# Performance work log

Hardware: AMD Instinct MI355X
Metric: run time of the kernel (lower is better)

## Reference

```python
import jax, jax.numpy as jnp
import numpy as np

B, T, D, L, S, SPAN = 16, 8192, 256, 256, 128, 64


def setup_inputs() -> dict:
    key = jax.random.key(0)
    k1, k2, k3, k4 = jax.random.split(key, 4)
    word_reps = jax.random.normal(k1, (B, T, D), dtype=jnp.float32)
    # contiguous non-overlapping spans of length SPAN covering each doc
    starts = jnp.arange(S, dtype=jnp.int32) * SPAN            # [S]
    ends = starts + SPAN                                      # [S]
    offsets = jnp.broadcast_to(jnp.stack([starts, ends], -1), (B, S, 2))
    W1 = jax.random.normal(k2, (D, L), dtype=jnp.float32) * (1.0 / np.sqrt(D))
    b1 = jax.random.normal(k3, (L,), dtype=jnp.float32) * 0.01
    v = jax.random.normal(k4, (L,), dtype=jnp.float32) * (1.0 / np.sqrt(L))
    return {"word_reps": word_reps, "offsets": offsets, "W1": W1, "b1": b1, "v": v}


def reference(word_reps, offsets, W1, b1, v):
    # alpha = v(start(word_reps)) : two stacked linears, no activation -> [B,T]
    alpha = jnp.einsum("btl,l->bt", jnp.einsum("btd,dl->btl", word_reps, W1) + b1, v)

    starts = offsets[..., 0]                                  # [B,S]
    ends = offsets[..., 1]                                    # [B,S]
    pos = jnp.arange(word_reps.shape[1], dtype=offsets.dtype) # [T]
    mask = (pos[None, None, :] >= starts[..., None]) & (pos[None, None, :] < ends[..., None])  # [B,S,T]

    # ragged per-span softmax over token axis
    neg_inf = jnp.asarray(-jnp.inf, dtype=alpha.dtype)
    scores = jnp.where(mask, alpha[:, None, :], neg_inf)      # [B,S,T]
    s = jax.nn.softmax(scores, axis=-1)                       # [B,S,T]

    # attention-weighted sum pooling per span
    span_rep = jnp.einsum("bst,btd->bsd", s, word_reps)       # [B,S,D]

    # span lengths phi and last-token reps
    phi = (ends - starts).astype(word_reps.dtype)[..., None]  # [B,S,1]
    batch_idx = jnp.arange(word_reps.shape[0])[:, None]       # [B,1]
    span_ends = word_reps[batch_idx, ends - 1]                # [B,S,D]

    final_span_rep = jnp.concatenate([span_ends, span_rep, phi], axis=-1)  # [B,S,2D+1]
    prop_lens = jnp.full((word_reps.shape[0],), offsets.shape[1], dtype=jnp.int32)
    return final_span_rep, prop_lens
```

## Files before the change

### kernel.cpp

```cpp
#include <hip/hip_runtime.h>
#include <math.h>

#define B_   16
#define T_   8192
#define D_   256
#define L_   256
#define S_   128

__global__ __launch_bounds__(64) void prep_weff(const float* __restrict__ W1,
                                                const float* __restrict__ v,
                                                float* __restrict__ weff) {
    int d    = blockIdx.x;
    int lane = threadIdx.x;
    const float4* w4 = reinterpret_cast<const float4*>(W1 + (size_t)d * L_);
    const float4* v4 = reinterpret_cast<const float4*>(v);
    float4 a = w4[lane];
    float4 b = v4[lane];
    float s = a.x * b.x + a.y * b.y + a.z * b.z + a.w * b.w;
#pragma unroll
    for (int off = 32; off; off >>= 1) s += __shfl_xor(s, off);
    if (lane == 0) weff[d] = s;
}

__global__ __launch_bounds__(256) void span_kernel(const float* __restrict__ wr,
                                                   const int*   __restrict__ offsets,
                                                   const float* __restrict__ weff,
                                                   float*       __restrict__ out) {
    const int tid  = threadIdx.x;
    const int wave = tid >> 6;
    const int lane = tid & 63;
    const int bs   = blockIdx.x * 4 + wave;
    const int b    = bs >> 7;
    const int sp   = bs & (S_ - 1);

    const int start = offsets[bs * 2 + 0];
    const int end   = offsets[bs * 2 + 1];
    const int len   = end - start;

    const int g  = lane >> 4;
    const int c0 = lane & 15;

    const float4* wf4 = reinterpret_cast<const float4*>(weff);
    const float4 we0 = wf4[c0];
    const float4 we1 = wf4[c0 + 16];
    const float4 we2 = wf4[c0 + 32];
    const float4 we3 = wf4[c0 + 48];

    float4 acc0 = make_float4(0.f, 0.f, 0.f, 0.f);
    float4 acc1 = make_float4(0.f, 0.f, 0.f, 0.f);
    float4 acc2 = make_float4(0.f, 0.f, 0.f, 0.f);
    float4 acc3 = make_float4(0.f, 0.f, 0.f, 0.f);
    float  z    = 0.f;

    const float* base = wr + (size_t)(b * T_ + start) * D_;

#pragma unroll 4
    for (int p = 0; p < 16; ++p) {
        const int t  = 4 * p + g;
        const int tc = (t < len) ? t : (len - 1);
        const float4* row = reinterpret_cast<const float4*>(base + (size_t)tc * D_);
        float4 x0 = row[c0];
        float4 x1 = row[c0 + 16];
        float4 x2 = row[c0 + 32];
        float4 x3 = row[c0 + 48];

        float s = x0.x * we0.x + x0.y * we0.y + x0.z * we0.z + x0.w * we0.w
                + x1.x * we1.x + x1.y * we1.y + x1.z * we1.z + x1.w * we1.w
                + x2.x * we2.x + x2.y * we2.y + x2.z * we2.z + x2.w * we2.w
                + x3.x * we3.x + x3.y * we3.y + x3.z * we3.z + x3.w * we3.w;
        s += __shfl_xor(s, 1);
        s += __shfl_xor(s, 2);
        s += __shfl_xor(s, 4);
        s += __shfl_xor(s, 8);

        const float e = (t < len) ? __expf(s) : 0.f;
        z += e;
        acc0.x += e * x0.x; acc0.y += e * x0.y; acc0.z += e * x0.z; acc0.w += e * x0.w;
        acc1.x += e * x1.x; acc1.y += e * x1.y; acc1.z += e * x1.z; acc1.w += e * x1.w;
        acc2.x += e * x2.x; acc2.y += e * x2.y; acc2.z += e * x2.z; acc2.w += e * x2.w;
        acc3.x += e * x3.x; acc3.y += e * x3.y; acc3.z += e * x3.z; acc3.w += e * x3.w;
    }

#pragma unroll
    for (int off = 16; off <= 32; off <<= 1) {
        z      += __shfl_xor(z, off);
        acc0.x += __shfl_xor(acc0.x, off); acc0.y += __shfl_xor(acc0.y, off);
        acc0.z += __shfl_xor(acc0.z, off); acc0.w += __shfl_xor(acc0.w, off);
        acc1.x += __shfl_xor(acc1.x, off); acc1.y += __shfl_xor(acc1.y, off);
        acc1.z += __shfl_xor(acc1.z, off); acc1.w += __shfl_xor(acc1.w, off);
        acc2.x += __shfl_xor(acc2.x, off); acc2.y += __shfl_xor(acc2.y, off);
        acc2.z += __shfl_xor(acc2.z, off); acc2.w += __shfl_xor(acc2.w, off);
        acc3.x += __shfl_xor(acc3.x, off); acc3.y += __shfl_xor(acc3.y, off);
        acc3.z += __shfl_xor(acc3.z, off); acc3.w += __shfl_xor(acc3.w, off);
    }
    const float inv = 1.f / z;

    const float4 sel = (g == 0) ? acc0 : (g == 1) ? acc1 : (g == 2) ? acc2 : acc3;

    const size_t o = (size_t)bs * (2 * D_ + 1);
    out[o + D_ + lane * 4 + 0] = sel.x * inv;
    out[o + D_ + lane * 4 + 1] = sel.y * inv;
    out[o + D_ + lane * 4 + 2] = sel.z * inv;
    out[o + D_ + lane * 4 + 3] = sel.w * inv;

    const float4* lrow =
        reinterpret_cast<const float4*>(wr + (size_t)(b * T_ + end - 1) * D_);
    const float4 le = lrow[lane];
    out[o + lane * 4 + 0] = le.x;
    out[o + lane * 4 + 1] = le.y;
    out[o + lane * 4 + 2] = le.z;
    out[o + lane * 4 + 3] = le.w;

    if (lane == 0) {
        out[o + 2 * D_] = (float)len;
        if (sp == 0) out[(size_t)B_ * S_ * (2 * D_ + 1) + b] = (float)S_;
    }
}

extern "C" void kernel_launch(void* const* d_in, const int* in_sizes, int n_in,
                              void* d_out, int out_size, void* d_ws, size_t ws_size,
                              hipStream_t stream) {
    const float* word_reps = (const float*)d_in[0];
    const int*   offsets   = (const int*)d_in[1];
    const float* W1        = (const float*)d_in[2];
    const float* v         = (const float*)d_in[4];
    float*       out       = (float*)d_out;
    float*       weff      = (float*)d_ws;

    prep_weff<<<D_, 64, 0, stream>>>(W1, v, weff);
    span_kernel<<<(B_ * S_) / 4, 256, 0, stream>>>(word_reps, offsets, weff, out);
}
```

Measured before the change: 33.97 us.

## Split each span across two waves and stage output rows through LDS

Each span is now handled by two waves, each covering half of its tokens, and the partial sums and normalizers are combined through shared memory. This doubles the grid and wave count so more loads are in flight on a bandwidth-bound kernel. Input rows are read with nontemporal loads. The output row is assembled in LDS and written with coalesced nontemporal stores instead of strided scalar stores. The cost is two block barriers and extra shared-memory traffic.

```diff
diff --git a/kernel.cpp b/kernel.cpp
--- a/kernel.cpp
+++ b/kernel.cpp
@@ -6,6 +6,8 @@
 #define D_   256
 #define L_   256
 #define S_   128
+
+typedef float floatx4 __attribute__((ext_vector_type(4)));
 
 __global__ __launch_bounds__(64) void prep_weff(const float* __restrict__ W1,
                                                 const float* __restrict__ v,
@@ -22,6 +24,11 @@
     if (lane == 0) weff[d] = s;
 }
 
+__device__ __forceinline__ float4 nt_load4(const float4* p) {
+    floatx4 r = __builtin_nontemporal_load(reinterpret_cast<const floatx4*>(p));
+    return make_float4(r.x, r.y, r.z, r.w);
+}
+
 __global__ __launch_bounds__(256) void span_kernel(const float* __restrict__ wr,
                                                    const int*   __restrict__ offsets,
                                                    const float* __restrict__ weff,
@@ -29,7 +36,9 @@
     const int tid  = threadIdx.x;
     const int wave = tid >> 6;
     const int lane = tid & 63;
-    const int bs   = blockIdx.x * 4 + wave;
+    const int sib  = wave >> 1;
+    const int wk   = wave & 1;
+    const int bs   = blockIdx.x * 2 + sib;
     const int b    = bs >> 7;
     const int sp   = bs & (S_ - 1);
 
@@ -54,15 +63,15 @@
 
     const float* base = wr + (size_t)(b * T_ + start) * D_;
 
-#pragma unroll 4
-    for (int p = 0; p < 16; ++p) {
-        const int t  = 4 * p + g;
+#pragma unroll
+    for (int p = 0; p < 8; ++p) {
+        const int t  = 32 * wk + 4 * p + g;
         const int tc = (t < len) ? t : (len - 1);
         const float4* row = reinterpret_cast<const float4*>(base + (size_t)tc * D_);
-        float4 x0 = row[c0];
-        float4 x1 = row[c0 + 16];
-        float4 x2 = row[c0 + 32];
-        float4 x3 = row[c0 + 48];
+        float4 x0 = nt_load4(row + c0);
+        float4 x1 = nt_load4(row + c0 + 16);
+        float4 x2 = nt_load4(row + c0 + 32);
+        float4 x3 = nt_load4(row + c0 + 48);
 
         float s = x0.x * we0.x + x0.y * we0.y + x0.z * we0.z + x0.w * we0.w
                 + x1.x * we1.x + x1.y * we1.y + x1.z * we1.z + x1.w * we1.w
@@ -93,26 +102,48 @@
         acc3.x += __shfl_xor(acc3.x, off); acc3.y += __shfl_xor(acc3.y, off);
         acc3.z += __shfl_xor(acc3.z, off); acc3.w += __shfl_xor(acc3.w, off);
     }
-    const float inv = 1.f / z;
 
     const float4 sel = (g == 0) ? acc0 : (g == 1) ? acc1 : (g == 2) ? acc2 : acc3;
 
+    __shared__ float4 sacc[4][64];
+    __shared__ float  szz[4];
+    __shared__ float  srow[2][513];
+
+    sacc[wave][lane] = sel;
+    if (lane == 0) szz[wave] = z;
+
+    float4 le = make_float4(0.f, 0.f, 0.f, 0.f);
+    if (wk == 0) {
+        const float4* lrow =
+            reinterpret_cast<const float4*>(wr + (size_t)(b * T_ + end - 1) * D_);
+        le = lrow[lane];
+    }
+    __syncthreads();
+
+    if (wk == 0) {
+        const float4 sA = sacc[2 * sib + 0][lane];
+        const float4 sB = sacc[2 * sib + 1][lane];
+        const float  inv = 1.f / (szz[2 * sib + 0] + szz[2 * sib + 1]);
+        srow[sib][lane * 4 + 0] = le.x;
+        srow[sib][lane * 4 + 1] = le.y;
+        srow[sib][lane * 4 + 2] = le.z;
+        srow[sib][lane * 4 + 3] = le.w;
+        srow[sib][256 + lane * 4 + 0] = (sA.x + sB.x) * inv;
+        srow[sib][256 + lane * 4 + 1] = (sA.y + sB.y) * inv;
+        srow[sib][256 + lane * 4 + 2] = (sA.z + sB.z) * inv;
+        srow[sib][256 + lane * 4 + 3] = (sA.w + sB.w) * inv;
+        if (lane == 0) srow[sib][512] = (float)len;
+    }
+    __syncthreads();
+
+    const int q = wk * 64 + lane;
     const size_t o = (size_t)bs * (2 * D_ + 1);
-    out[o + D_ + lane * 4 + 0] = sel.x * inv;
-    out[o + D_ + lane * 4 + 1] = sel.y * inv;
-    out[o + D_ + lane * 4 + 2] = sel.z * inv;
-    out[o + D_ + lane * 4 + 3] = sel.w * inv;
-
-    const float4* lrow =
-        reinterpret_cast<const float4*>(wr + (size_t)(b * T_ + end - 1) * D_);
-    const float4 le = lrow[lane];
-    out[o + lane * 4 + 0] = le.x;
-    out[o + lane * 4 + 1] = le.y;
-    out[o + lane * 4 + 2] = le.z;
-    out[o + lane * 4 + 3] = le.w;
-
-    if (lane == 0) {
-        out[o + 2 * D_] = (float)len;
+#pragma unroll
+    for (int k = 0; k < 4; ++k) {
+        __builtin_nontemporal_store(srow[sib][q + 128 * k], &out[o + q + 128 * k]);
+    }
+    if (q == 0) {
+        out[o + 512] = srow[sib][512];
         if (sp == 0) out[(size_t)B_ * S_ * (2 * D_ + 1) + b] = (float)S_;
     }
 }
@@ -128,5 +159,5 @@
     float*       weff      = (float*)d_ws;
 
     prep_weff<<<D_, 64, 0, stream>>>(W1, v, weff);
-    span_kernel<<<(B_ * S_) / 4, 256, 0, stream>>>(word_reps, offsets, weff, out);
+    span_kernel<<<(B_ * S_) / 2, 256, 0, stream>>>(word_reps, offsets, weff, out);
 }
```

Measured after the change: 29.92 us. 1.14x faster.

## Give each span its own 4-wave block and reduce partials through LDS

Applied to the files above, without the earlier changes.

Each block now handles one span instead of four. Each of the 4 waves processes 16 tokens, with every lane holding one float4 of a full 256-wide row, so the per-token dot product becomes a full-wave shuffle reduction. Per-wave partial softmax numerators and denominators are combined through shared memory. The last-token row is taken from the registers of the final wave, which avoids a second global read. Input rows are read with nontemporal loads and output is written with coalesced per-thread nontemporal stores; the trade-off is more blocks and two barriers per span.

```diff
diff --git a/kernel.cpp b/kernel.cpp
--- a/kernel.cpp
+++ b/kernel.cpp
@@ -6,6 +6,8 @@
 #define D_   256
 #define L_   256
 #define S_   128
+
+typedef float floatx4 __attribute__((ext_vector_type(4)));
 
 __global__ __launch_bounds__(64) void prep_weff(const float* __restrict__ W1,
                                                 const float* __restrict__ v,
@@ -22,14 +24,19 @@
     if (lane == 0) weff[d] = s;
 }
 
-__global__ __launch_bounds__(256) void span_kernel(const float* __restrict__ wr,
-                                                   const int*   __restrict__ offsets,
-                                                   const float* __restrict__ weff,
-                                                   float*       __restrict__ out) {
+__device__ __forceinline__ float4 nt_load4(const float* p) {
+    floatx4 r = __builtin_nontemporal_load(reinterpret_cast<const floatx4*>(p));
+    return make_float4(r.x, r.y, r.z, r.w);
+}
+
+__global__ __launch_bounds__(256, 8) void span_kernel(const float* __restrict__ wr,
+                                                      const int*   __restrict__ offsets,
+                                                      const float* __restrict__ weff,
+                                                      float*       __restrict__ out) {
     const int tid  = threadIdx.x;
     const int wave = tid >> 6;
     const int lane = tid & 63;
-    const int bs   = blockIdx.x * 4 + wave;
+    const int bs   = blockIdx.x;
     const int b    = bs >> 7;
     const int sp   = bs & (S_ - 1);
 
@@ -37,82 +44,60 @@
     const int end   = offsets[bs * 2 + 1];
     const int len   = end - start;
 
-    const int g  = lane >> 4;
-    const int c0 = lane & 15;
+    const float4 we = reinterpret_cast<const float4*>(weff)[lane];
 
-    const float4* wf4 = reinterpret_cast<const float4*>(weff);
-    const float4 we0 = wf4[c0];
-    const float4 we1 = wf4[c0 + 16];
-    const float4 we2 = wf4[c0 + 32];
-    const float4 we3 = wf4[c0 + 48];
-
-    float4 acc0 = make_float4(0.f, 0.f, 0.f, 0.f);
-    float4 acc1 = make_float4(0.f, 0.f, 0.f, 0.f);
-    float4 acc2 = make_float4(0.f, 0.f, 0.f, 0.f);
-    float4 acc3 = make_float4(0.f, 0.f, 0.f, 0.f);
-    float  z    = 0.f;
+    float4 acc = make_float4(0.f, 0.f, 0.f, 0.f);
+    float  z   = 0.f;
+    float4 x   = make_float4(0.f, 0.f, 0.f, 0.f);
 
     const float* base = wr + (size_t)(b * T_ + start) * D_;
 
-#pragma unroll 4
+#pragma unroll
     for (int p = 0; p < 16; ++p) {
-        const int t  = 4 * p + g;
+        const int t  = wave * 16 + p;
         const int tc = (t < len) ? t : (len - 1);
-        const float4* row = reinterpret_cast<const float4*>(base + (size_t)tc * D_);
-        float4 x0 = row[c0];
-        float4 x1 = row[c0 + 16];
-        float4 x2 = row[c0 + 32];
-        float4 x3 = row[c0 + 48];
+        x = nt_load4(base + (size_t)tc * D_ + lane * 4);
 
-        float s = x0.x * we0.x + x0.y * we0.y + x0.z * we0.z + x0.w * we0.w
-                + x1.x * we1.x + x1.y * we1.y + x1.z * we1.z + x1.w * we1.w
-                + x2.x * we2.x + x2.y * we2.y + x2.z * we2.z + x2.w * we2.w
-                + x3.x * we3.x + x3.y * we3.y + x3.z * we3.z + x3.w * we3.w;
+        float s = x.x * we.x + x.y * we.y + x.z * we.z + x.w * we.w;
         s += __shfl_xor(s, 1);
         s += __shfl_xor(s, 2);
         s += __shfl_xor(s, 4);
         s += __shfl_xor(s, 8);
+        s += __shfl_xor(s, 16);
+        s += __shfl_xor(s, 32);
 
         const float e = (t < len) ? __expf(s) : 0.f;
         z += e;
-        acc0.x += e * x0.x; acc0.y += e * x0.y; acc0.z += e * x0.z; acc0.w += e * x0.w;
-        acc1.x += e * x1.x; acc1.y += e * x1.y; acc1.z += e * x1.z; acc1.w += e * x1.w;
-        acc2.x += e * x2.x; acc2.y += e * x2.y; acc2.z += e * x2.z; acc2.w += e * x2.w;
-        acc3.x += e * x3.x; acc3.y += e * x3.y; acc3.z += e * x3.z; acc3.w += e * x3.w;
+        acc.x += e * x.x;
+        acc.y += e * x.y;
+        acc.z += e * x.z;
+        acc.w += e * x.w;
     }
 
-#pragma unroll
-    for (int off = 16; off <= 32; off <<= 1) {
-        z      += __shfl_xor(z, off);
-        acc0.x += __shfl_xor(acc0.x, off); acc0.y += __shfl_xor(acc0.y, off);
-        acc0.z += __shfl_xor(acc0.z, off); acc0.w += __shfl_xor(acc0.w, off);
-        acc1.x += __shfl_xor(acc1.x, off); acc1.y += __shfl_xor(acc1.y, off);
-        acc1.z += __shfl_xor(acc1.z, off); acc1.w += __shfl_xor(acc1.w, off);
-        acc2.x += __shfl_xor(acc2.x, off); acc2.y += __shfl_xor(acc2.y, off);
-        acc2.z += __shfl_xor(acc2.z, off); acc2.w += __shfl_xor(acc2.w, off);
-        acc3.x += __shfl_xor(acc3.x, off); acc3.y += __shfl_xor(acc3.y, off);
-        acc3.z += __shfl_xor(acc3.z, off); acc3.w += __shfl_xor(acc3.w, off);
+    __shared__ float4 sacc[4][64];
+    __shared__ float  szz[4];
+    __shared__ float  srow[512];
+
+    sacc[wave][lane] = acc;
+    if (lane == 0) szz[wave] = z;
+    if (wave == 3) {
+        srow[lane * 4 + 0] = x.x;
+        srow[lane * 4 + 1] = x.y;
+        srow[lane * 4 + 2] = x.z;
+        srow[lane * 4 + 3] = x.w;
     }
-    const float inv = 1.f / z;
+    __syncthreads();
 
-    const float4 sel = (g == 0) ? acc0 : (g == 1) ? acc1 : (g == 2) ? acc2 : acc3;
+    const float inv = 1.f / (szz[0] + szz[1] + szz[2] + szz[3]);
+    const float* sa = reinterpret_cast<const float*>(sacc);
+    srow[256 + tid] = (sa[tid] + sa[256 + tid] + sa[512 + tid] + sa[768 + tid]) * inv;
+    __syncthreads();
 
     const size_t o = (size_t)bs * (2 * D_ + 1);
-    out[o + D_ + lane * 4 + 0] = sel.x * inv;
-    out[o + D_ + lane * 4 + 1] = sel.y * inv;
-    out[o + D_ + lane * 4 + 2] = sel.z * inv;
-    out[o + D_ + lane * 4 + 3] = sel.w * inv;
-
-    const float4* lrow =
-        reinterpret_cast<const float4*>(wr + (size_t)(b * T_ + end - 1) * D_);
-    const float4 le = lrow[lane];
-    out[o + lane * 4 + 0] = le.x;
-    out[o + lane * 4 + 1] = le.y;
-    out[o + lane * 4 + 2] = le.z;
-    out[o + lane * 4 + 3] = le.w;
-
-    if (lane == 0) {
-        out[o + 2 * D_] = (float)len;
+    __builtin_nontemporal_store(srow[tid],       &out[o + tid]);
+    __builtin_nontemporal_store(srow[256 + tid], &out[o + 256 + tid]);
+    if (tid == 0) {
+        out[o + 512] = (float)len;
         if (sp == 0) out[(size_t)B_ * S_ * (2 * D_ + 1) + b] = (float)S_;
     }
 }
@@ -128,5 +113,5 @@
     float*       weff      = (float*)d_ws;
 
     prep_weff<<<D_, 64, 0, stream>>>(W1, v, weff);
-    span_kernel<<<(B_ * S_) / 4, 256, 0, stream>>>(word_reps, offsets, weff, out);
+    span_kernel<<<B_ * S_, 256, 0, stream>>>(word_reps, offsets, weff, out);
 }
```

New measurement: 31.39 us. -7.6%, faster.
